# Optimization experiments

Measured on AMD Instinct MI355X. Metric: run time of the kernel, lower is better.

Reference implementation:

```python
import jax, jax.numpy as jnp
import numpy as np

N = 20480          # total points (single cloud, batch id 0)
C = 64             # in_channels
K = 16             # neighbors
CHUNK = 512        # knn_batch_size: query chunk for cdist
BN_EPS = 1e-5
# grid_size_options: [tower, background, line] x 3 axes
GRID_OPTIONS = np.array([[0.05, 0.05, 0.05],
                         [0.20, 0.20, 0.20],
                         [0.10, 0.10, 0.10]], dtype=np.float32)


def setup_inputs() -> dict:
    key = jax.random.key(0)
    k1, k2, k3, k4 = jax.random.split(key, 4)
    feat = jax.random.normal(k1, (N, C), jnp.float32)
    coord = jax.random.uniform(k2, (N, 3), jnp.float32)
    batch = jnp.zeros((N,), jnp.int32)
    fj_w1 = jax.random.normal(k3, (C, 32), jnp.float32) * 0.05
    fj_b1 = jnp.zeros((32,), jnp.float32)
    bn_gamma = jnp.ones((32,), jnp.float32)
    bn_beta = jnp.zeros((32,), jnp.float32)
    fj_w2 = jax.random.normal(k4, (32, 3), jnp.float32) * 0.05
    fj_b2 = jnp.zeros((3,), jnp.float32)
    return {"feat": feat, "coord": coord, "batch": batch,
            "fj_w1": fj_w1, "fj_b1": fj_b1, "bn_gamma": bn_gamma,
            "bn_beta": bn_beta, "fj_w2": fj_w2, "fj_b2": fj_b2}


def reference(feat, coord, batch, fj_w1, fj_b1, bn_gamma, bn_beta, fj_w2, fj_b2):
    # ---- chunked brute-force KNN (cdist + topk, self excluded) ----
    sq_all = jnp.sum(coord * coord, axis=-1)            # [N]
    col = jnp.arange(N)
    coords_chunks = coord.reshape(-1, CHUNK, 3)
    idx_chunks = jnp.arange(N).reshape(-1, CHUNK)

    def knn_chunk(args):
        cq, qi = args                                   # [CHUNK,3], [CHUNK]
        d2 = (jnp.sum(cq * cq, -1)[:, None] + sq_all[None, :]
              - 2.0 * (cq @ coord.T))                   # [CHUNK, N]
        d2 = jnp.maximum(d2, 1e-12)
        d2 = jnp.where(col[None, :] == qi[:, None], jnp.inf, d2)
        neg, idx = jax.lax.top_k(-d2, K)                # smallest-K (sqrt monotone)
        return jnp.sqrt(-neg), idx

    dists, idxs = jax.lax.map(jax.checkpoint(knn_chunk), (coords_chunks, idx_chunks))
    all_dist = dists.reshape(N, K)                      # [N, K]
    all_idx = idxs.reshape(N, K)                        # [N, K]

    # ---- per-point covariance of neighbor coords + 3x3 SVD (local PCA) ----
    nb = coord[all_idx]                                 # [N, K, 3]
    nc = nb - nb.mean(axis=1, keepdims=True)
    cov = jnp.einsum('nkd,nke->nde', nc, nc) / (K - 1)  # [N, 3, 3]
    S = jnp.linalg.svd(cov, compute_uv=False)           # descending, [N, 3]
    S_norm = S / (S.sum(axis=1, keepdims=True) + 1e-6)
    linearity = (S_norm[:, 0] - (S_norm[:, 1] + S_norm[:, 2]))[:, None]  # [N,1]

    mean_dist = all_dist.mean(axis=1, keepdims=True)
    density = 1.0 / (mean_dist + 1e-6)

    # ---- feature_judge MLP: Linear -> BatchNorm1d (train stats) -> ReLU -> Linear ----
    h = feat @ fj_w1 + fj_b1
    mu = h.mean(axis=0)
    var = h.var(axis=0)  # biased, as torch BN uses for normalization
    h = (h - mu) / jnp.sqrt(var + BN_EPS) * bn_gamma + bn_beta
    h = jax.nn.relu(h)
    probs = jax.nn.softmax(h @ fj_w2 + fj_b2, axis=1)   # [N, 3]

    tower_prob = (density * 2.0 + probs[:, 0:1]) / 3.0
    background_prob = (jnp.maximum(1.0 - linearity, 1.0 - density) + probs[:, 1:2]) / 3.0
    line_prob = (linearity * 2.0 + probs[:, 2:3]) / 3.0

    go = jnp.asarray(GRID_OPTIONS)
    line_grid = go[2] * jnp.array([1.0, 1.0, 5.0], jnp.float32)  # z-axis line grid *5
    grids = (tower_prob * go[0][None, :] + background_prob * go[1][None, :]
             + line_prob * line_grid[None, :] + 1e-6)   # [N, 3]
    return grids
```

## Files before the change

### kernel.cpp

```cpp
#include <hip/hip_runtime.h>

#define NPTS   20480
#define KNN    16
#define NSLOT  20
#define NCH    32
#define NFEAT  64
#define BN_EPS 1e-5f
#define AMB_EPS 2.6e-7f
#define GH     16
#define NCELL  (GH*GH*GH)
#define RHO0   2
#define NBLK   (NPTS / 256)
#define MLPBLK 640
#define MLPGRID (NPTS / 64)
#define NGRP   (NPTS / 64)
#define NWAVE  4
#define NPAR   4

__device__ __forceinline__ unsigned med3u(unsigned a, unsigned b, unsigned c) {
    unsigned d;
    asm("v_med3_u32 %0, %1, %2, %3" : "=v"(d) : "v"(a), "v"(b), "v"(c));
    return d;
}

__device__ __forceinline__ float ref_d2_raw(float qx, float qy, float qz, float sqq,
                                            float cx, float cy, float cz, float sqc) {
    float dot = fmaf(qz, cz, fmaf(qy, cy, __fmul_rn(qx, cx)));
    float t   = __fadd_rn(sqq, sqc);
    return fmaf(-2.0f, dot, t);
}
__device__ __forceinline__ float ref_d2(float qx, float qy, float qz, float sqq,
                                        float cx, float cy, float cz, float sqc) {
    return fmaxf(ref_d2_raw(qx, qy, qz, sqq, cx, cy, cz, sqc), 1e-12f);
}

template <int STEP>
__device__ __forceinline__ void scan_range(const float4* __restrict__ spts,
                                           int c0, int c1, float4 qp, int self,
                                           unsigned* b) {
    for (int c = c0; c < c1; c += STEP) {
        float4 s = spts[c];
        float d2 = ref_d2_raw(qp.x, qp.y, qp.z, qp.w, s.x, s.y, s.z, s.w);
        unsigned key = (__float_as_uint(d2) & 0xFFFF8000u) | (unsigned)c;
        if (c == self) key = 0xFFFFFFFFu;
#pragma unroll
        for (int s2 = NSLOT - 1; s2 >= 1; --s2) b[s2] = med3u(key, b[s2 - 1], b[s2]);
        b[0] = min(key, b[0]);
    }
}

__global__ __launch_bounds__(256) void zero_cells(int* __restrict__ p) {
    p[blockIdx.x * 256 + threadIdx.x] = 0;
}

__global__ __launch_bounds__(256) void prep_mlp(const float* __restrict__ coord,
                                                float4* __restrict__ pts4,
                                                int* __restrict__ pcell,
                                                int* __restrict__ cnt,
                                                const float* __restrict__ feat,
                                                const float* __restrict__ w1,
                                                const float* __restrict__ b1,
                                                float* __restrict__ h_ws,
                                                float* __restrict__ partials) {
    __shared__ float sfeat[64 * 65];
    __shared__ float hpart[4][64][NCH + 1];
    const int tid = threadIdx.x;

    if (blockIdx.x < NBLK) {
        int i = blockIdx.x * 256 + tid;
        float x = coord[3 * i + 0], y = coord[3 * i + 1], z = coord[3 * i + 2];
        float sq = __fadd_rn(__fadd_rn(__fmul_rn(x, x), __fmul_rn(y, y)),
                             __fmul_rn(z, z));
        pts4[i] = make_float4(x, y, z, sq);
        int ix = min(GH - 1, max(0, (int)(x * (float)GH)));
        int iy = min(GH - 1, max(0, (int)(y * (float)GH)));
        int iz = min(GH - 1, max(0, (int)(z * (float)GH)));
        int cell = (iz * GH + iy) * GH + ix;
        pcell[i] = cell;
        atomicAdd(&cnt[cell], 1);
        return;
    }
    const int blk  = blockIdx.x - NBLK;
    const int lane = tid & 63;
    const int wv   = __builtin_amdgcn_readfirstlane(tid >> 6);

    const float4* fsrc = reinterpret_cast<const float4*>(feat + (size_t)blk * 64 * NFEAT);
#pragma unroll
    for (int it = 0; it < 4; ++it) {
        float4 v = fsrc[it * 256 + tid];
        int f = it * 1024 + tid * 4;
        int pt = f >> 6, c = f & 63;
        sfeat[pt * 65 + c + 0] = v.x;
        sfeat[pt * 65 + c + 1] = v.y;
        sfeat[pt * 65 + c + 2] = v.z;
        sfeat[pt * 65 + c + 3] = v.w;
    }
    __syncthreads();

    float hA[NCH], hB[NCH];
#pragma unroll
    for (int j = 0; j < NCH; ++j) { hA[j] = 0.f; hB[j] = 0.f; }
    const int cbase = wv * 16;
#pragma unroll
    for (int cc = 0; cc < 16; ++cc) {
        int c = cbase + cc;
        float fv = sfeat[lane * 65 + c];
        const float* wrow = w1 + c * NCH;
        if (cc < 8) {
#pragma unroll
            for (int j = 0; j < NCH; ++j) hA[j] = fmaf(fv, wrow[j], hA[j]);
        } else {
#pragma unroll
            for (int j = 0; j < NCH; ++j) hB[j] = fmaf(fv, wrow[j], hB[j]);
        }
    }
#pragma unroll
    for (int j = 0; j < NCH; ++j) hpart[wv][lane][j] = hA[j] + hB[j];
    __syncthreads();
    if (wv != 0) return;

    float h[NCH];
#pragma unroll
    for (int j = 0; j < NCH; ++j) {
        float q0 = hpart[0][lane][j], q1 = hpart[1][lane][j];
        float q2 = hpart[2][lane][j], q3 = hpart[3][lane][j];
        h[j] = (q0 + q1) + (q2 + q3) + 0.f;
        h[j] = h[j] + b1[j];
    }
    float4* hd = reinterpret_cast<float4*>(h_ws + ((size_t)blk * 64 + lane) * NCH);
#pragma unroll
    for (int j4 = 0; j4 < NCH / 4; ++j4)
        hd[j4] = make_float4(h[4 * j4], h[4 * j4 + 1], h[4 * j4 + 2], h[4 * j4 + 3]);

    float myS0 = 0.f, myQ0 = 0.f, myS1 = 0.f, myQ1 = 0.f;
#pragma unroll
    for (int j = 0; j < NCH; ++j) {
        float v = h[j], vv = h[j] * h[j];
        v += __shfl_xor(v, 1, 64);  vv += __shfl_xor(vv, 1, 64);
        v += __shfl_xor(v, 2, 64);  vv += __shfl_xor(vv, 2, 64);
        v += __shfl_xor(v, 4, 64);  vv += __shfl_xor(vv, 4, 64);
        float t0 = __shfl(v, 0, 64),  t1 = __shfl(v, 8, 64);
        float t2 = __shfl(v, 16, 64), t3 = __shfl(v, 24, 64);
        float t4 = __shfl(v, 32, 64), t5 = __shfl(v, 40, 64);
        float t6 = __shfl(v, 48, 64), t7 = __shfl(v, 56, 64);
        float u0 = __shfl(vv, 0, 64),  u1 = __shfl(vv, 8, 64);
        float u2 = __shfl(vv, 16, 64), u3 = __shfl(vv, 24, 64);
        float u4 = __shfl(vv, 32, 64), u5 = __shfl(vv, 40, 64);
        float u6 = __shfl(vv, 48, 64), u7 = __shfl(vv, 56, 64);
        float s0 = ((t0 + t1) + t2) + t3;
        float s1 = ((t4 + t5) + t6) + t7;
        float q0 = ((u0 + u1) + u2) + u3;
        float q1 = ((u4 + u5) + u6) + u7;
        if (lane == j) { myS0 = s0; myQ0 = q0; myS1 = s1; myQ1 = q1; }
    }
    if (lane < NCH) {
        partials[(size_t)(2 * blk) * 64 + lane]            = myS0;
        partials[(size_t)(2 * blk) * 64 + NCH + lane]      = myQ0;
        partials[(size_t)(2 * blk + 1) * 64 + lane]        = myS1;
        partials[(size_t)(2 * blk + 1) * 64 + NCH + lane]  = myQ1;
    }
}

__global__ __launch_bounds__(256) void scatter_pref(const float4* __restrict__ pts4,
                                                    const int* __restrict__ pcell,
                                                    const int* __restrict__ cnt,
                                                    int* __restrict__ cursor,
                                                    float4* __restrict__ spts,
                                                    int* __restrict__ sidx,
                                                    const float* __restrict__ partials,
                                                    float* __restrict__ mustats,
                                                    int* __restrict__ startArr) {
    const int tid = threadIdx.x;
    const int lane = tid & 63;
    if (blockIdx.x < NBLK) {
        __shared__ int chunks[256];
        __shared__ int sstart[NCELL];
        int local[16];
        int base = tid * 16, s = 0;
#pragma unroll
        for (int i = 0; i < 16; ++i) { local[i] = cnt[base + i]; s += local[i]; }
        chunks[tid] = s;
        __syncthreads();
        if (tid < 64) {
            int a0 = chunks[4 * tid + 0], a1 = chunks[4 * tid + 1];
            int a2 = chunks[4 * tid + 2], a3 = chunks[4 * tid + 3];
            int tot = a0 + a1 + a2 + a3;
            int inc = tot;
#pragma unroll
            for (int d = 1; d < 64; d <<= 1) {
                int t = __shfl_up(inc, d, 64);
                if (lane >= d) inc += t;
            }
            int excl = inc - tot;
            chunks[4 * tid + 0] = excl;
            chunks[4 * tid + 1] = excl + a0;
            chunks[4 * tid + 2] = excl + a0 + a1;
            chunks[4 * tid + 3] = excl + a0 + a1 + a2;
        }
        __syncthreads();
        int acc = chunks[tid];
#pragma unroll
        for (int i = 0; i < 16; ++i) { sstart[base + i] = acc; acc += local[i]; }
        __syncthreads();
        int i = blockIdx.x * 256 + tid;
        int c = pcell[i];
        int slot = sstart[c] + atomicAdd(&cursor[c], 1);
        spts[slot] = pts4[i];
        sidx[slot] = i;
        return;
    }
    if (tid < 64) {
        double s = 0.0;
        for (int bk = 0; bk < MLPBLK; ++bk) s += (double)partials[bk * 64 + lane];
        __shared__ double smu[NCH];
        if (lane < NCH) { double mu = s / (double)NPTS; smu[lane] = mu; mustats[lane] = (float)mu; }
        __syncthreads();
        if (lane >= NCH) {
            int jj = lane - NCH;
            double var = s / (double)NPTS - smu[jj] * smu[jj];
            mustats[lane] = (float)(1.0 / sqrt(var + (double)BN_EPS));
        }
    } else if (tid < 128) {
        __syncthreads();
        int base = lane * (NCELL / 64);
        int tot = 0;
        for (int i = 0; i < NCELL / 64; ++i) tot += cnt[base + i];
        int inc = tot;
#pragma unroll
        for (int d = 1; d < 64; d <<= 1) {
            int t = __shfl_up(inc, d, 64);
            if (lane >= d) inc += t;
        }
        int acc = inc - tot;
        for (int i = 0; i < NCELL / 64; ++i) { startArr[base + i] = acc; acc += cnt[base + i]; }
        if (lane == 63) startArr[NCELL] = acc;
    } else {
        __syncthreads();
    }
}

__global__ __launch_bounds__(256) void knn_scan(
    const float4* __restrict__ spts, const int* __restrict__ start,
    unsigned* __restrict__ quarterkeys) {
    __shared__ unsigned keysh[NWAVE * NSLOT][64];
    const int lane = threadIdx.x & 63;
    const int wv   = threadIdx.x >> 6;
    const int g    = blockIdx.x >> 2;
    const int par  = blockIdx.x & 3;
    const int slot = g * 64 + lane;
    const float4 qp = spts[slot];
    const int ix = min(GH - 1, max(0, (int)(qp.x * (float)GH)));
    const int iy = min(GH - 1, max(0, (int)(qp.y * (float)GH)));
    const int iz = min(GH - 1, max(0, (int)(qp.z * (float)GH)));

    unsigned b[NSLOT];
#pragma unroll
    for (int s = 0; s < NSLOT; ++s) b[s] = 0xFFFFFFFFu;
    {
        const int zlo = max(0, iz - RHO0), zhi = min(GH - 1, iz + RHO0);
        const int ylo = max(0, iy - RHO0), yhi = min(GH - 1, iy + RHO0);
        const int xlo = max(0, ix - RHO0), xhi = min(GH - 1, ix + RHO0);
        int r = 0;
        for (int cz = zlo; cz <= zhi; ++cz)
            for (int cy = ylo; cy <= yhi; ++cy) {
                if ((r & (NWAVE - 1)) == wv) {
                    const int rb = (cz * GH + cy) * GH;
                    int c0 = start[rb + xlo];
                    int c1 = start[rb + xhi + 1];
                    scan_range<NPAR>(spts, c0 + ((par - c0) & (NPAR - 1)), c1,
                                     qp, slot, b);
                }
                ++r;
            }
    }
#pragma unroll
    for (int s = 0; s < NSLOT; ++s) keysh[wv * NSLOT + s][lane] = b[s];
    __syncthreads();

    unsigned m[NSLOT];
    if (wv < 2) {
#pragma unroll
        for (int s = 0; s < NSLOT; ++s) m[s] = 0xFFFFFFFFu;
        for (int p2 = 2 * wv; p2 <= 2 * wv + 1; ++p2) {
#pragma unroll
            for (int s = 0; s < NSLOT; ++s) {
                unsigned key = keysh[p2 * NSLOT + s][lane];
#pragma unroll
                for (int t = NSLOT - 1; t >= 1; --t) m[t] = med3u(key, m[t - 1], m[t]);
                m[0] = min(key, m[0]);
            }
        }
    }
    __syncthreads();
    if (wv < 2) {
#pragma unroll
        for (int s = 0; s < NSLOT; ++s) keysh[wv * NSLOT + s][lane] = m[s];
    }
    __syncthreads();
    if (wv != 0) return;

#pragma unroll
    for (int s = 0; s < NSLOT; ++s) m[s] = 0xFFFFFFFFu;
    for (int p2 = 0; p2 < 2; ++p2) {
#pragma unroll
        for (int s = 0; s < NSLOT; ++s) {
            unsigned key = keysh[p2 * NSLOT + s][lane];
#pragma unroll
            for (int t = NSLOT - 1; t >= 1; --t) m[t] = med3u(key, m[t - 1], m[t]);
            m[0] = min(key, m[0]);
        }
    }
    unsigned* myh = quarterkeys + (size_t)(g * NPAR + par) * NSLOT * 64;
#pragma unroll
    for (int s = 0; s < NSLOT; ++s) myh[s * 64 + lane] = m[s];
}

__device__ void knn_stats(const float4* __restrict__ spts,
                          double qx, double qy, double qz,
                          const int* idx, const float* d2s,
                          double* den_out, double* lin_out) {
    double sx = 0, sy = 0, sz = 0;
    double sxx = 0, syy = 0, szz = 0, sxy = 0, sxz = 0, syz = 0;
    double dsum = 0;
#pragma unroll
    for (int s = 0; s < KNN; ++s) {
        float4 cp = spts[idx[s]];
        double ax = (double)cp.x - qx;
        double ay = (double)cp.y - qy;
        double az = (double)cp.z - qz;
        sx += ax; sy += ay; sz += az;
        sxx += ax * ax; syy += ay * ay; szz += az * az;
        sxy += ax * ay; sxz += ax * az; syz += ay * az;
        dsum += (double)sqrtf(d2s[s]);
    }
    const double invK  = 1.0 / KNN;
    const double invK1 = 1.0 / (KNN - 1);
    double mxx = sx * invK, myy = sy * invK, mzz = sz * invK;
    double cxx = (sxx - (double)KNN * mxx * mxx) * invK1;
    double cyy = (syy - (double)KNN * myy * myy) * invK1;
    double czz = (szz - (double)KNN * mzz * mzz) * invK1;
    double cxy = (sxy - (double)KNN * mxx * myy) * invK1;
    double cxz = (sxz - (double)KNN * mxx * mzz) * invK1;
    double cyz = (syz - (double)KNN * myy * mzz) * invK1;

    double T  = cxx + cyy + czz;
    double qq = T / 3.0;
    double b00 = cxx - qq, b11 = cyy - qq, b22 = czz - qq;
    double p2 = b00 * b00 + b11 * b11 + b22 * b22
              + 2.0 * (cxy * cxy + cxz * cxz + cyz * cyz);
    double lmax;
    if (p2 <= 1e-30) {
        lmax = qq;
    } else {
        double p = sqrt(p2 / 6.0);
        double detB = b00 * (b11 * b22 - cyz * cyz)
                    - cxy * (cxy * b22 - cyz * cxz)
                    + cxz * (cxy * cyz - b11 * cxz);
        double r = detB / (2.0 * p * p * p);
        r = fmin(1.0, fmax(-1.0, r));
        double phi = acos(r) / 3.0;
        lmax = qq + 2.0 * p * cos(phi);
    }
    *lin_out = (2.0 * lmax - T) / (T + 1e-6);
    *den_out = 1.0 / (dsum * invK + 1e-6);
}

__global__ __launch_bounds__(64) void knn_finalize(
    const float4* __restrict__ spts, const int* __restrict__ sidx,
    const int* __restrict__ start,   const unsigned* __restrict__ quarterkeys,
    const float* __restrict__ h_ws,  const float* __restrict__ gamma,
    const float* __restrict__ beta,  const float* __restrict__ w2,
    const float* __restrict__ b2,    const float* __restrict__ mustats,
    float* __restrict__ out) {
    const int lane = threadIdx.x;
    const int g    = blockIdx.x;
    const int slot = g * 64 + lane;
    const float4 qp = spts[slot];
    const int ix = min(GH - 1, max(0, (int)(qp.x * (float)GH)));
    const int iy = min(GH - 1, max(0, (int)(qp.y * (float)GH)));
    const int iz = min(GH - 1, max(0, (int)(qp.z * (float)GH)));

    unsigned m[NSLOT];
#pragma unroll
    for (int s = 0; s < NSLOT; ++s) m[s] = 0xFFFFFFFFu;
    for (int par = 0; par < NPAR; ++par) {
        const unsigned* ph = quarterkeys + (size_t)(g * NPAR + par) * NSLOT * 64;
#pragma unroll
        for (int s = 0; s < NSLOT; ++s) {
            unsigned key = ph[s * 64 + lane];
#pragma unroll
            for (int t = NSLOT - 1; t >= 1; --t) m[t] = med3u(key, m[t - 1], m[t]);
            m[0] = min(key, m[0]);
        }
    }

    const float h = 1.0f / (float)GH;
    int rho = RHO0;
    for (;;) {
        float b16f = __uint_as_float(m[16] & 0xFFFF8000u);
        float cov  = (float)(rho * rho) * (h * h);
        bool ok = (fmaf(b16f, 0.00390625f, b16f) + 1e-6f) <= cov;
        if (__all(ok) || rho >= GH - 1) break;
        ++rho;
        if (!ok) {
#pragma unroll
            for (int s = 0; s < NSLOT; ++s) m[s] = 0xFFFFFFFFu;
            const int zlo = max(0, iz - rho), zhi = min(GH - 1, iz + rho);
            const int ylo = max(0, iy - rho), yhi = min(GH - 1, iy + rho);
            const int xlo = max(0, ix - rho), xhi = min(GH - 1, ix + rho);
            for (int cz = zlo; cz <= zhi; ++cz)
                for (int cy = ylo; cy <= yhi; ++cy) {
                    const int rb = (cz * GH + cy) * GH;
                    scan_range<1>(spts, start[rb + xlo], start[rb + xhi + 1],
                                  qp, slot, m);
                }
        }
    }

    unsigned long long gk[KNN + 1];
#pragma unroll
    for (int s = 0; s < KNN + 1; ++s) gk[s] = ~0ull;
#pragma unroll
    for (int s = 0; s < NSLOT; ++s) {
        unsigned bs = m[s];
        int cs = min((int)(bs & 0x7FFFu), NPTS - 1);
        float4 cp = spts[cs];
        float d2 = ref_d2(qp.x, qp.y, qp.z, qp.w, cp.x, cp.y, cp.z, cp.w);
        unsigned long long kk =
            ((unsigned long long)__float_as_uint(d2) << 32) | (unsigned)cs;
        if (bs == 0xFFFFFFFFu) kk = ~0ull;
#pragma unroll
        for (int t = KNN; t >= 1; --t) {
            unsigned long long mn = (kk < gk[t]) ? kk : gk[t];
            gk[t] = (gk[t - 1] > mn) ? gk[t - 1] : mn;
        }
        gk[0] = (kk < gk[0]) ? kk : gk[0];
    }

    int   idxA[KNN];
    float d2A[KNN];
#pragma unroll
    for (int s = 0; s < KNN; ++s) {
        idxA[s] = (int)(gk[s] & 0xFFFFFFFFull);
        d2A[s]  = __uint_as_float((unsigned)(gk[s] >> 32));
    }
    float d16 = d2A[KNN - 1];
    float d17 = __uint_as_float((unsigned)(gk[KNN] >> 32));
    bool amb = (__fsub_rn(d17, d16) <= AMB_EPS);

    const double qx = (double)qp.x, qy = (double)qp.y, qz = (double)qp.z;
    double denA, linA;
    knn_stats(spts, qx, qy, qz, idxA, d2A, &denA, &linA);
    double den = denA, lin_d = linA;
    if (amb) {
        idxA[KNN - 1] = (int)(gk[KNN] & 0xFFFFFFFFull);
        d2A[KNN - 1]  = d17;
        double denB, linB;
        knn_stats(spts, qx, qy, qz, idxA, d2A, &denB, &linB);
        den = 0.5 * (denA + denB);
        lin_d = 0.5 * (linA + linB);
    }
    float dens = (float)den;
    float lin  = (float)lin_d;

    const int qi = sidx[slot];
    float hh[NCH];
    const float4* h4 = reinterpret_cast<const float4*>(h_ws + (size_t)qi * NCH);
#pragma unroll
    for (int j4 = 0; j4 < NCH / 4; ++j4) {
        float4 v = h4[j4];
        hh[j4 * 4 + 0] = v.x; hh[j4 * 4 + 1] = v.y;
        hh[j4 * 4 + 2] = v.z; hh[j4 * 4 + 3] = v.w;
    }
    float l0 = b2[0], l1 = b2[1], l2 = b2[2];
#pragma unroll
    for (int j = 0; j < NCH; ++j) {
        float xn = (hh[j] - mustats[j]) * mustats[NCH + j] * gamma[j] + beta[j];
        xn = fmaxf(xn, 0.f);
        l0 = fmaf(xn, w2[j * 3 + 0], l0);
        l1 = fmaf(xn, w2[j * 3 + 1], l1);
        l2 = fmaf(xn, w2[j * 3 + 2], l2);
    }
    float mx = fmaxf(l0, fmaxf(l1, l2));
    float e0 = expf(l0 - mx), e1 = expf(l1 - mx), e2 = expf(l2 - mx);
    float is = 1.f / (e0 + e1 + e2);
    float p0 = e0 * is, p1 = e1 * is, p2v = e2 * is;

    float tower = (dens * 2.f + p0) * (1.f / 3.f);
    float back  = (fmaxf(1.f - lin, 1.f - dens) + p1) * (1.f / 3.f);
    float line  = (lin * 2.f + p2v) * (1.f / 3.f);
    float gxy = fmaf(tower, 0.05f, fmaf(back, 0.20f, fmaf(line, 0.10f, 1e-6f)));
    float gz  = fmaf(tower, 0.05f, fmaf(back, 0.20f, fmaf(line, 0.50f, 1e-6f)));
    out[3 * qi + 0] = gxy;
    out[3 * qi + 1] = gxy;
    out[3 * qi + 2] = gz;
}

extern "C" void kernel_launch(void* const* d_in, const int* in_sizes, int n_in,
                              void* d_out, int out_size, void* d_ws, size_t ws_size,
                              hipStream_t stream) {
    const float* feat  = (const float*)d_in[0];
    const float* coord = (const float*)d_in[1];
    const float* w1    = (const float*)d_in[3];
    const float* b1    = (const float*)d_in[4];
    const float* gamma = (const float*)d_in[5];
    const float* beta  = (const float*)d_in[6];
    const float* w2    = (const float*)d_in[7];
    const float* b2    = (const float*)d_in[8];
    float* out = (float*)d_out;

    float4* pts4   = (float4*)d_ws;
    float4* spts   = pts4 + NPTS;
    int* sidx      = (int*)(spts + NPTS);
    int* pcell     = sidx + NPTS;
    int* cnt       = pcell + NPTS;
    int* cursor    = cnt + NCELL;
    int* startArr  = cursor + NCELL;
    unsigned* quarterkeys = (unsigned*)(startArr + NCELL + 8);
    float* partials  = (float*)(quarterkeys + (size_t)NPAR * NGRP * NSLOT * 64);
    float* mustats   = partials + MLPBLK * 64;
    float* h_ws      = mustats + 64;

    zero_cells<<<(2 * NCELL) / 256, 256, 0, stream>>>(cnt);
    prep_mlp<<<NBLK + MLPGRID, 256, 0, stream>>>(coord, pts4, pcell, cnt,
                                                 feat, w1, b1, h_ws, partials);
    scatter_pref<<<NBLK + 1, 256, 0, stream>>>(pts4, pcell, cnt, cursor,
                                               spts, sidx, partials, mustats,
                                               startArr);
    knn_scan<<<NPAR * NGRP, 256, 0, stream>>>(spts, startArr, quarterkeys);
    knn_finalize<<<NGRP, 64, 0, stream>>>(spts, sidx, startArr, quarterkeys,
                                          h_ws, gamma, beta, w2, b2, mustats,
                                          out);
}
```

Before: 87.87 us.

## Fuse KNN scan and finalize via last-block-done atomic counter per group

Merges the knn_scan and knn_finalize kernels into one launch. Each of the four partial blocks per query group writes its candidate keys, fences, and bumps a per-group atomic counter. The last block to arrive merges the other partitions' keys and runs the finalize stage (refinement, PCA stats, MLP output). This removes a kernel launch and the device-wide barrier between the two stages. In exchange it adds fences and atomics, and the finalize tail now runs on one wave of a 256-thread block. The counters are zeroed by extending the existing zero_cells kernel.

```diff
diff --git a/kernel.cpp b/kernel.cpp
--- a/kernel.cpp
+++ b/kernel.cpp
@@ -16,6 +16,7 @@
 #define NGRP   (NPTS / 64)
 #define NWAVE  4
 #define NPAR   4
+#define NZERO  (2 * NCELL + NGRP)
 
 __device__ __forceinline__ unsigned med3u(unsigned a, unsigned b, unsigned c) {
     unsigned d;
@@ -50,7 +51,8 @@
 }
 
 __global__ __launch_bounds__(256) void zero_cells(int* __restrict__ p) {
-    p[blockIdx.x * 256 + threadIdx.x] = 0;
+    int i = blockIdx.x * 256 + threadIdx.x;
+    if (i < NZERO) p[i] = 0;
 }
 
 __global__ __launch_bounds__(256) void prep_mlp(const float* __restrict__ coord,
@@ -124,7 +126,7 @@
     for (int j = 0; j < NCH; ++j) {
         float q0 = hpart[0][lane][j], q1 = hpart[1][lane][j];
         float q2 = hpart[2][lane][j], q3 = hpart[3][lane][j];
-        h[j] = (q0 + q1) + (q2 + q3) + 0.f;
+        h[j] = (q0 + q1) + (q2 + q3);
         h[j] = h[j] + b1[j];
     }
     float4* hd = reinterpret_cast<float4*>(h_ws + ((size_t)blk * 64 + lane) * NCH);
@@ -239,9 +241,64 @@
     }
 }
 
-__global__ __launch_bounds__(256) void knn_scan(
-    const float4* __restrict__ spts, const int* __restrict__ start,
-    unsigned* __restrict__ quarterkeys) {
+__device__ void knn_stats(const float4* __restrict__ spts,
+                          double qx, double qy, double qz,
+                          const int* idx, const float* d2s,
+                          double* den_out, double* lin_out) {
+    double sx = 0, sy = 0, sz = 0;
+    double sxx = 0, syy = 0, szz = 0, sxy = 0, sxz = 0, syz = 0;
+    double dsum = 0;
+#pragma unroll
+    for (int s = 0; s < KNN; ++s) {
+        float4 cp = spts[idx[s]];
+        double ax = (double)cp.x - qx;
+        double ay = (double)cp.y - qy;
+        double az = (double)cp.z - qz;
+        sx += ax; sy += ay; sz += az;
+        sxx += ax * ax; syy += ay * ay; szz += az * az;
+        sxy += ax * ay; sxz += ax * az; syz += ay * az;
+        dsum += (double)sqrtf(d2s[s]);
+    }
+    const double invK  = 1.0 / KNN;
+    const double invK1 = 1.0 / (KNN - 1);
+    double mxx = sx * invK, myy = sy * invK, mzz = sz * invK;
+    double cxx = (sxx - (double)KNN * mxx * mxx) * invK1;
+    double cyy = (syy - (double)KNN * myy * myy) * invK1;
+    double czz = (szz - (double)KNN * mzz * mzz) * invK1;
+    double cxy = (sxy - (double)KNN * mxx * myy) * invK1;
+    double cxz = (sxz - (double)KNN * mxx * mzz) * invK1;
+    double cyz = (syz - (double)KNN * myy * mzz) * invK1;
+
+    double T  = cxx + cyy + czz;
+    double qq = T / 3.0;
+    double b00 = cxx - qq, b11 = cyy - qq, b22 = czz - qq;
+    double p2 = b00 * b00 + b11 * b11 + b22 * b22
+              + 2.0 * (cxy * cxy + cxz * cxz + cyz * cyz);
+    double lmax;
+    if (p2 <= 1e-30) {
+        lmax = qq;
+    } else {
+        double p = sqrt(p2 / 6.0);
+        double detB = b00 * (b11 * b22 - cyz * cyz)
+                    - cxy * (cxy * b22 - cyz * cxz)
+                    + cxz * (cxy * cyz - b11 * cxz);
+        double r = detB / (2.0 * p * p * p);
+        r = fmin(1.0, fmax(-1.0, r));
+        double phi = acos(r) / 3.0;
+        lmax = qq + 2.0 * p * cos(phi);
+    }
+    *lin_out = (2.0 * lmax - T) / (T + 1e-6);
+    *den_out = 1.0 / (dsum * invK + 1e-6);
+}
+
+__global__ __launch_bounds__(256) void knn_fused(
+    const float4* __restrict__ spts, const int* __restrict__ sidx,
+    const int* __restrict__ start,   unsigned* __restrict__ quarterkeys,
+    int* __restrict__ flag,
+    const float* __restrict__ h_ws,  const float* __restrict__ gamma,
+    const float* __restrict__ beta,  const float* __restrict__ w2,
+    const float* __restrict__ b2,    const float* __restrict__ mustats,
+    float* __restrict__ out) {
     __shared__ unsigned keysh[NWAVE * NSLOT][64];
     const int lane = threadIdx.x & 63;
     const int wv   = threadIdx.x >> 6;
@@ -310,81 +367,20 @@
             m[0] = min(key, m[0]);
         }
     }
+
     unsigned* myh = quarterkeys + (size_t)(g * NPAR + par) * NSLOT * 64;
 #pragma unroll
     for (int s = 0; s < NSLOT; ++s) myh[s * 64 + lane] = m[s];
-}
-
-__device__ void knn_stats(const float4* __restrict__ spts,
-                          double qx, double qy, double qz,
-                          const int* idx, const float* d2s,
-                          double* den_out, double* lin_out) {
-    double sx = 0, sy = 0, sz = 0;
-    double sxx = 0, syy = 0, szz = 0, sxy = 0, sxz = 0, syz = 0;
-    double dsum = 0;
-#pragma unroll
-    for (int s = 0; s < KNN; ++s) {
-        float4 cp = spts[idx[s]];
-        double ax = (double)cp.x - qx;
-        double ay = (double)cp.y - qy;
-        double az = (double)cp.z - qz;
-        sx += ax; sy += ay; sz += az;
-        sxx += ax * ax; syy += ay * ay; szz += az * az;
-        sxy += ax * ay; sxz += ax * az; syz += ay * az;
-        dsum += (double)sqrtf(d2s[s]);
-    }
-    const double invK  = 1.0 / KNN;
-    const double invK1 = 1.0 / (KNN - 1);
-    double mxx = sx * invK, myy = sy * invK, mzz = sz * invK;
-    double cxx = (sxx - (double)KNN * mxx * mxx) * invK1;
-    double cyy = (syy - (double)KNN * myy * myy) * invK1;
-    double czz = (szz - (double)KNN * mzz * mzz) * invK1;
-    double cxy = (sxy - (double)KNN * mxx * myy) * invK1;
-    double cxz = (sxz - (double)KNN * mxx * mzz) * invK1;
-    double cyz = (syz - (double)KNN * myy * mzz) * invK1;
-
-    double T  = cxx + cyy + czz;
-    double qq = T / 3.0;
-    double b00 = cxx - qq, b11 = cyy - qq, b22 = czz - qq;
-    double p2 = b00 * b00 + b11 * b11 + b22 * b22
-              + 2.0 * (cxy * cxy + cxz * cxz + cyz * cyz);
-    double lmax;
-    if (p2 <= 1e-30) {
-        lmax = qq;
-    } else {
-        double p = sqrt(p2 / 6.0);
-        double detB = b00 * (b11 * b22 - cyz * cyz)
-                    - cxy * (cxy * b22 - cyz * cxz)
-                    + cxz * (cxy * cyz - b11 * cxz);
-        double r = detB / (2.0 * p * p * p);
-        r = fmin(1.0, fmax(-1.0, r));
-        double phi = acos(r) / 3.0;
-        lmax = qq + 2.0 * p * cos(phi);
-    }
-    *lin_out = (2.0 * lmax - T) / (T + 1e-6);
-    *den_out = 1.0 / (dsum * invK + 1e-6);
-}
-
-__global__ __launch_bounds__(64) void knn_finalize(
-    const float4* __restrict__ spts, const int* __restrict__ sidx,
-    const int* __restrict__ start,   const unsigned* __restrict__ quarterkeys,
-    const float* __restrict__ h_ws,  const float* __restrict__ gamma,
-    const float* __restrict__ beta,  const float* __restrict__ w2,
-    const float* __restrict__ b2,    const float* __restrict__ mustats,
-    float* __restrict__ out) {
-    const int lane = threadIdx.x;
-    const int g    = blockIdx.x;
-    const int slot = g * 64 + lane;
-    const float4 qp = spts[slot];
-    const int ix = min(GH - 1, max(0, (int)(qp.x * (float)GH)));
-    const int iy = min(GH - 1, max(0, (int)(qp.y * (float)GH)));
-    const int iz = min(GH - 1, max(0, (int)(qp.z * (float)GH)));
-
-    unsigned m[NSLOT];
-#pragma unroll
-    for (int s = 0; s < NSLOT; ++s) m[s] = 0xFFFFFFFFu;
-    for (int par = 0; par < NPAR; ++par) {
-        const unsigned* ph = quarterkeys + (size_t)(g * NPAR + par) * NSLOT * 64;
+    __threadfence();
+    int old = 0;
+    if (lane == 0) old = atomicAdd(&flag[g], 1);
+    old = __shfl(old, 0, 64);
+    if (old != NPAR - 1) return;
+    __threadfence();
+
+    for (int p2 = 0; p2 < NPAR; ++p2) {
+        if (p2 == par) continue;
+        const unsigned* ph = quarterkeys + (size_t)(g * NPAR + p2) * NSLOT * 64;
 #pragma unroll
         for (int s = 0; s < NSLOT; ++s) {
             unsigned key = ph[s * 64 + lane];
@@ -515,20 +511,20 @@
     int* pcell     = sidx + NPTS;
     int* cnt       = pcell + NPTS;
     int* cursor    = cnt + NCELL;
-    int* startArr  = cursor + NCELL;
+    int* flag      = cursor + NCELL;
+    int* startArr  = flag + NGRP;
     unsigned* quarterkeys = (unsigned*)(startArr + NCELL + 8);
     float* partials  = (float*)(quarterkeys + (size_t)NPAR * NGRP * NSLOT * 64);
     float* mustats   = partials + MLPBLK * 64;
     float* h_ws      = mustats + 64;
 
-    zero_cells<<<(2 * NCELL) / 256, 256, 0, stream>>>(cnt);
+    zero_cells<<<(NZERO + 255) / 256, 256, 0, stream>>>(cnt);
     prep_mlp<<<NBLK + MLPGRID, 256, 0, stream>>>(coord, pts4, pcell, cnt,
                                                  feat, w1, b1, h_ws, partials);
     scatter_pref<<<NBLK + 1, 256, 0, stream>>>(pts4, pcell, cnt, cursor,
                                                spts, sidx, partials, mustats,
                                                startArr);
-    knn_scan<<<NPAR * NGRP, 256, 0, stream>>>(spts, startArr, quarterkeys);
-    knn_finalize<<<NGRP, 64, 0, stream>>>(spts, sidx, startArr, quarterkeys,
-                                          h_ws, gamma, beta, w2, b2, mustats,
-                                          out);
-}
+    knn_fused<<<NPAR * NGRP, 256, 0, stream>>>(spts, sidx, startArr, quarterkeys,
+                                               flag, h_ws, gamma, beta, w2, b2,
+                                               mustats, out);
+}
```

Result: slower. 152.5 us (+73.6%).
